# Kernel tuning notes

Hardware: AMD Instinct MI355X
Metric: run time of the kernel (lower is better)

The kernel has to match this reference:

```python
import jax, jax.numpy as jnp
import numpy as np
from jax import lax

B, DIM, RES = 1024, 384, 7
HEADS, KEY_DIM, ATTN_RATIO = 8, 32, 4
N = RES * RES            # 49
KH = KEY_DIM * HEADS     # 256
D = ATTN_RATIO * KEY_DIM # 128
DH = D * HEADS           # 1024
SCALE = KEY_DIM ** -0.5


def _rel_pos_idx():
    ii, jj = np.meshgrid(np.arange(RES), np.arange(RES), indexing='ij')
    pos = np.stack([ii.ravel(), jj.ravel()])          # [2, N]
    rel = np.abs(pos[:, :, None] - pos[:, None, :])   # [2, N, N]
    return jnp.asarray(rel[0] * RES + rel[1])         # [N, N] int

REL_IDX = _rel_pos_idx()


def conv1x1_bn(x, w, b, s, o):
    # 1x1 conv (pointwise GEMM) + eval-mode BatchNorm folded to scale/shift
    y = jnp.einsum('oc,bchw->bohw', w, x) + b[:, None, None]
    return y * s[:, None, None] + o[:, None, None]


def setup_inputs() -> dict:
    key = jax.random.key(0)
    ks = jax.random.split(key, 32)
    f = lambda i, shape, scale=0.02: jax.random.normal(ks[i], shape, jnp.float32) * scale
    u = lambda i, shape: jax.random.uniform(ks[i], shape, jnp.float32, 0.5, 1.5)
    inp = {
        'x': jax.random.normal(ks[0], (B, DIM, RES, RES), jnp.float32),
        'q_w': f(1, (KH, DIM)), 'q_b': f(2, (KH,)), 'q_s': u(3, (KH,)), 'q_o': f(4, (KH,)),
        'k_w': f(5, (KH, DIM)), 'k_b': f(6, (KH,)), 'k_s': u(7, (KH,)), 'k_o': f(8, (KH,)),
        'v_w': f(9, (DH, DIM)), 'v_b': f(10, (DH,)), 'v_s': u(11, (DH,)), 'v_o': f(12, (DH,)),
        'vl_w': f(13, (DH, 1, 3, 3)), 'vl_b': f(14, (DH,)), 'vl_s': u(15, (DH,)), 'vl_o': f(16, (DH,)),
        'th1_w': f(17, (HEADS, HEADS), 0.1), 'th1_b': f(18, (HEADS,)),
        'th2_w': f(19, (HEADS, HEADS), 0.1), 'th2_b': f(20, (HEADS,)),
        'p_w': f(21, (DIM, DH)), 'p_b': f(22, (DIM,)), 'p_s': u(23, (DIM,)), 'p_o': f(24, (DIM,)),
        'ab': f(25, (HEADS, N), 0.1),
    }
    return inp


def reference(x, q_w, q_b, q_s, q_o, k_w, k_b, k_s, k_o, v_w, v_b, v_s, v_o,
              vl_w, vl_b, vl_s, vl_o, th1_w, th1_b, th2_w, th2_b,
              p_w, p_b, p_s, p_o, ab):
    b = x.shape[0]
    q = conv1x1_bn(x, q_w, q_b, q_s, q_o).reshape(b, HEADS, KEY_DIM, N)
    q = q.transpose(0, 1, 3, 2)                         # [B,H,N,kd]
    k = conv1x1_bn(x, k_w, k_b, k_s, k_o).reshape(b, HEADS, KEY_DIM, N)  # [B,H,kd,N]
    v4 = conv1x1_bn(x, v_w, v_b, v_s, v_o)              # [B,DH,7,7]
    # local depthwise 3x3 branch + BN
    vl = lax.conv_general_dilated(v4, vl_w, (1, 1), 'SAME',
                                  feature_group_count=DH,
                                  dimension_numbers=('NCHW', 'OIHW', 'NCHW'))
    vl = (vl + vl_b[:, None, None]) * vl_s[:, None, None] + vl_o[:, None, None]
    v = v4.reshape(b, HEADS, D, N).transpose(0, 1, 3, 2)  # [B,H,N,d]

    bias = ab[:, REL_IDX]                                # [H,N,N]
    attn = jnp.einsum('bhnd,bhdm->bhnm', q, k) * SCALE + bias[None]
    # talking head 1 (1x1 conv over head dim)
    attn = jnp.einsum('ij,bjnm->binm', th1_w, attn) + th1_b[None, :, None, None]
    attn = jax.nn.softmax(attn, axis=-1)
    # talking head 2
    attn = jnp.einsum('ij,bjnm->binm', th2_w, attn) + th2_b[None, :, None, None]

    out = jnp.einsum('bhnm,bhmd->bhnd', attn, v)         # [B,H,N,d]
    out = out.transpose(0, 1, 3, 2).reshape(b, DH, RES, RES) + vl
    out = jax.nn.gelu(out, approximate=False)            # nn.GELU default = exact
    out = conv1x1_bn(out, p_w, p_b, p_s, p_o)            # [B,DIM,7,7]
    return out
```

## Files before the change

kernel.cpp:

```cpp
#include <hip/hip_runtime.h>
#include <math.h>

typedef unsigned short u16;
typedef unsigned int u32;
typedef short short8 __attribute__((ext_vector_type(8)));
typedef float f32x4 __attribute__((ext_vector_type(4)));
typedef unsigned int u32x2 __attribute__((ext_vector_type(2)));

#define SCALE_QK 0.17677669529663687f
#define PSLAB 23296

__device__ __forceinline__ float b2f(u16 v) { return __uint_as_float(((u32)v) << 16); }
__device__ __forceinline__ u16 f2b(float f) {
  u32 u = __float_as_uint(f);
  return (u16)((u + 0x7fffu + ((u >> 16) & 1u)) >> 16);
}

__device__ __forceinline__ float gelu_f(float z) {
  float y = z * 0.70710678118654752f;
  float a = fabsf(y);
  float t = __builtin_amdgcn_rcpf(fmaf(0.3275911f, a, 1.0f));
  float e = __expf(-y * y);
  float p = fmaf(1.061405429f, t, -1.453152027f);
  p = fmaf(p, t, 1.421413741f);
  p = fmaf(p, t, -0.284496736f);
  p = fmaf(p, t, 0.254829592f);
  p = p * t * e;
  float phi = (y >= 0.f) ? fmaf(-0.5f, p, 1.0f) : 0.5f * p;
  return z * phi;
}

__global__ __launch_bounds__(256) void k_pre(
    const float* __restrict__ th1w, const float* __restrict__ th1b, const float* __restrict__ ab,
    const float* __restrict__ qb, const float* __restrict__ qs, const float* __restrict__ qo,
    const float* __restrict__ kb, const float* __restrict__ ks, const float* __restrict__ ko,
    const float* __restrict__ vb, const float* __restrict__ vs, const float* __restrict__ vo,
    const float* __restrict__ pb, const float* __restrict__ ps, const float* __restrict__ po,
    const float* __restrict__ qw, const float* __restrict__ kw,
    const float* __restrict__ vw, const float* __restrict__ pw,
    float* __restrict__ bias2, float* __restrict__ alpha, float* __restrict__ beta,
    float* __restrict__ alphap, float* __restrict__ betap,
    u16* __restrict__ Wqk, u16* __restrict__ Wv, u16* __restrict__ Wp)
{
  int gid = blockIdx.x * 256 + threadIdx.x;
  if (gid < 19208) {
    int i = gid / 2401, rem = gid % 2401, n = rem / 49, m = rem % 49;
    int ry = abs(n / 7 - m / 7), rx = abs(n % 7 - m % 7);
    int idx = ry * 7 + rx;
    float acc = th1b[i];
    #pragma unroll
    for (int j = 0; j < 8; j++) acc += th1w[i * 8 + j] * ab[j * 49 + idx];
    bias2[gid] = acc;
  } else if (gid < 20744) {
    int c = gid - 19208;
    const float *s, *bb, *oo; int idx;
    if (c < 256)      { s = qs; bb = qb; oo = qo; idx = c; }
    else if (c < 512) { s = ks; bb = kb; oo = ko; idx = c - 256; }
    else              { s = vs; bb = vb; oo = vo; idx = c - 512; }
    float sv = s[idx];
    alpha[c] = sv;
    beta[c] = sv * bb[idx] + oo[idx];
  } else if (gid < 21128) {
    int c = gid - 20744;
    float sv = ps[c];
    alphap[c] = sv;
    betap[c] = sv * pb[c] + po[c];
  } else {
    int g = gid - 21128;
    if (g < 98304)       Wqk[g] = f2b(qw[g]);
    else if (g < 196608) Wqk[g] = f2b(kw[g - 98304]);
    else if (g < 589824) Wv[g - 196608] = f2b(vw[g - 196608]);
    else if (g < 983040) Wp[g - 589824] = f2b(pw[g - 589824]);
  }
}

__global__ __launch_bounds__(512, 4) void k_qk(
    const float* __restrict__ x, const u16* __restrict__ Wqk,
    const float* __restrict__ alpha, const float* __restrict__ beta,
    u16* __restrict__ Pbuf)
{
  __shared__ __align__(16) u16 lds[37376];
  u16* XT = lds;
  u16* Tq = lds + 26112;
  u16* Tk = lds + 31744;
  int t = threadIdx.x, wv = t >> 6, l = t & 63, quad = l >> 4, l16 = l & 15;
  int b = blockIdx.x;
  const float* xb = x + (size_t)b * 18816;

  for (int e = t; e < 18816; e += 512) {
    int k = e / 49, n = e - k * 49;
    XT[n * 408 + k] = f2b(xb[e]);
  }
  for (int e = t; e < 3060; e += 512) {
    int r = e / 204, kk = e - r * 204;
    ((u32*)(XT + (49 + r) * 408))[kk] = 0;
  }
  __syncthreads();

  u16* Pg = Pbuf + (size_t)b * PSLAB;
  int isK = wv >= 4, wl = wv & 3;
  for (int hp = 0; hp < 4; hp++) {
    int cbase = (isK ? 256 : 0) + hp * 64 + wl * 16;
    f32x4 acc[4] = {};
    const u16* Wr = Wqk + (size_t)(cbase + l16) * 384;
    short8 afr[12];
    #pragma unroll
    for (int ks = 0; ks < 12; ks++) afr[ks] = *(const short8*)(Wr + ks * 32 + quad * 8);
    #pragma unroll
    for (int ks = 0; ks < 12; ks++) {
      #pragma unroll
      for (int nt = 0; nt < 4; nt++) {
        short8 bf = *(const short8*)(&XT[(nt * 16 + l16) * 408 + ks * 32 + quad * 8]);
        acc[nt] = __builtin_amdgcn_mfma_f32_16x16x32_bf16(afr[ks], bf, acc[nt], 0, 0, 0);
      }
    }
    u16* Tdst = isK ? Tk : Tq;
    #pragma unroll
    for (int reg = 0; reg < 4; reg++) {
      int c = cbase + quad * 4 + reg;
      float al = alpha[c], be = beta[c];
      int cl = wl * 16 + quad * 4 + reg;
      #pragma unroll
      for (int nt = 0; nt < 4; nt++)
        Tdst[(nt * 16 + l16) * 88 + cl] = f2b(acc[nt][reg] * al + be);
    }
    __syncthreads();
    #pragma unroll
    for (int ui = 0; ui < 4; ui++) {
      int u = wv * 4 + ui;
      int hl = u >> 4, tn = (u >> 2) & 3, tm = u & 3;
      short8 a  = *(const short8*)(&Tq[(tn * 16 + l16) * 88 + hl * 32 + quad * 8]);
      short8 bb = *(const short8*)(&Tk[(tm * 16 + l16) * 88 + hl * 32 + quad * 8]);
      f32x4 c = {};
      c = __builtin_amdgcn_mfma_f32_16x16x32_bf16(a, bb, c, 0, 0, 0);
      int h = hp * 2 + hl;
      #pragma unroll
      for (int r = 0; r < 4; r++) {
        int n = tn * 16 + quad * 4 + r, m = tm * 16 + l16;
        if (n < 52 && m < 56)
          Pg[(h * 52 + n) * 56 + m] = (n < 49 && m < 49) ? f2b(c[r] * SCALE_QK) : (u16)0;
      }
    }
    __syncthreads();
  }
}

__global__ __launch_bounds__(256, 4) void k_mix(
    u16* __restrict__ Pbuf, const float* __restrict__ bias2,
    const float* __restrict__ th1w, const float* __restrict__ th1b,
    const float* __restrict__ th2w, const float* __restrict__ th2b)
{
  __shared__ u16 SB[23296];
  __shared__ float TH[144];
  int t = threadIdx.x, b = blockIdx.x;
  u32* Pg32 = (u32*)(Pbuf + (size_t)b * PSLAB);
  for (int e = t; e < 11648; e += 256) ((u32*)SB)[e] = Pg32[e];
  if (t < 64)       TH[t] = th1w[t];
  else if (t < 72)  TH[t] = th1b[t - 64];
  else if (t < 136) TH[t] = th2w[t - 72];
  else if (t < 144) TH[t] = th2b[t - 136];
  __syncthreads();
  for (int e = t; e < 2401; e += 256) {
    int n = e / 49, m = e - n * 49;
    float s[8], uo[8];
    #pragma unroll
    for (int j = 0; j < 8; j++) s[j] = b2f(SB[(j * 52 + n) * 56 + m]);
    #pragma unroll
    for (int i = 0; i < 8; i++) {
      float a2 = bias2[(i * 49 + n) * 49 + m];
      #pragma unroll
      for (int j = 0; j < 8; j++) a2 += TH[i * 8 + j] * s[j];
      uo[i] = a2;
    }
    #pragma unroll
    for (int i = 0; i < 8; i++) SB[(i * 52 + n) * 56 + m] = f2b(uo[i]);
  }
  __syncthreads();
  for (int r0 = t; r0 < 392; r0 += 256) {
    int i = r0 / 49, n = r0 - i * 49;
    u16* row = &SB[(i * 52 + n) * 56];
    float v[49]; float mx = -1e30f;
    #pragma unroll
    for (int m = 0; m < 49; m++) { v[m] = b2f(row[m]); mx = fmaxf(mx, v[m]); }
    float sum = 0.f;
    #pragma unroll
    for (int m = 0; m < 49; m++) { v[m] = __expf(v[m] - mx); sum += v[m]; }
    float inv = 1.f / sum;
    #pragma unroll
    for (int m = 0; m < 49; m++) row[m] = f2b(v[m] * inv);
  }
  __syncthreads();
  for (int e = t; e < 2401; e += 256) {
    int n = e / 49, m = e - n * 49;
    float s[8], uo[8];
    #pragma unroll
    for (int j = 0; j < 8; j++) s[j] = b2f(SB[(j * 52 + n) * 56 + m]);
    #pragma unroll
    for (int i = 0; i < 8; i++) {
      float a2 = TH[136 + i];
      #pragma unroll
      for (int j = 0; j < 8; j++) a2 += TH[72 + i * 8 + j] * s[j];
      uo[i] = a2;
    }
    #pragma unroll
    for (int i = 0; i < 8; i++) SB[(i * 52 + n) * 56 + m] = f2b(uo[i]);
  }
  __syncthreads();
  for (int e = t; e < 11648; e += 256) Pg32[e] = ((u32*)SB)[e];
}

__global__ __launch_bounds__(512, 4) void k_av(
    const float* __restrict__ x, const u16* __restrict__ Wv,
    const float* __restrict__ alpha, const float* __restrict__ beta,
    const float* __restrict__ vlw, const float* __restrict__ vlb,
    const float* __restrict__ vls, const float* __restrict__ vlo,
    const u16* __restrict__ Pbuf, u16* __restrict__ Zs)
{
  __shared__ __align__(16) u16 lds[38968];
  u16* XT = lds;
  u16* VT = lds + 26112;
  u16* Ph = lds + 35328;
  int t = threadIdx.x, wv = t >> 6, l = t & 63, quad = l >> 4, l16 = l & 15;
  int b = blockIdx.x;
  const float* xb = x + (size_t)b * 18816;

  for (int e = t; e < 18816; e += 512) {
    int k = e / 49, n = e - k * 49;
    XT[n * 408 + k] = f2b(xb[e]);
  }
  for (int e = t; e < 3060; e += 512) {
    int r = e / 204, kk = e - r * 204;
    ((u32*)(XT + (49 + r) * 408))[kk] = 0;
  }
  for (int e = t; e < 4608; e += 512) ((u32*)VT)[e] = 0;
  __syncthreads();

  u16* Zb = Zs + (size_t)b * 50176;
  const u16* Pgb = Pbuf + (size_t)b * PSLAB;
  for (int h = 0; h < 8; h++) {
    {
      const u32* src = (const u32*)(Pgb + h * 2912);
      for (int e = t; e < 1456; e += 512) ((u32*)Ph)[e] = src[e];
    }
    const u16* Wr = Wv + (size_t)(h * 128 + wv * 16 + l16) * 384;
    short8 afr[12];
    #pragma unroll
    for (int ks = 0; ks < 12; ks++) afr[ks] = *(const short8*)(Wr + ks * 32 + quad * 8);
    int d = wv * 16 + l16, c = h * 128 + d;
    float w9[9];
    #pragma unroll
    for (int j = 0; j < 9; j++) w9[j] = vlw[c * 9 + j];
    float sv = vls[c];
    float cb = sv * vlb[c] + vlo[c];

    f32x4 va[4] = {};
    #pragma unroll
    for (int ks = 0; ks < 12; ks++) {
      #pragma unroll
      for (int nt = 0; nt < 4; nt++) {
        short8 bf = *(const short8*)(&XT[(nt * 16 + l16) * 408 + ks * 32 + quad * 8]);
        va[nt] = __builtin_amdgcn_mfma_f32_16x16x32_bf16(afr[ks], bf, va[nt], 0, 0, 0);
      }
    }
    #pragma unroll
    for (int reg = 0; reg < 4; reg++) {
      int dl = wv * 16 + quad * 4 + reg;
      int cc = h * 128 + dl;
      float al = alpha[512 + cc], be = beta[512 + cc];
      #pragma unroll
      for (int nt = 0; nt < 4; nt++) {
        int m = nt * 16 + l16;
        if (m < 49) VT[dl * 72 + 8 + m] = f2b(va[nt][reg] * al + be);
      }
    }
    __syncthreads();
    f32x4 oa[4] = {};
    #pragma unroll
    for (int ks2 = 0; ks2 < 2; ks2++) {
      int mb = ks2 * 32 + quad * 8;
      short8 bf = *(const short8*)(&VT[(wv * 16 + l16) * 72 + 8 + mb]);
      #pragma unroll
      for (int tn = 0; tn < 4; tn++) {
        short8 af = *(const short8*)(&Ph[(tn * 16 + l16) * 56 + mb]);
        oa[tn] = __builtin_amdgcn_mfma_f32_16x16x32_bf16(af, bf, oa[tn], 0, 0, 0);
      }
    }
    const u16* vtr = &VT[d * 72];
    #pragma unroll
    for (int tn = 0; tn < 4; tn++) {
      int n0 = tn * 16 + quad * 4;
      const u16* vr = vtr + n0;
      float q[20];
      #pragma unroll
      for (int jj = 0; jj < 5; jj++) {
        u32x2 U = *(const u32x2*)(vr + jj * 4);
        q[jj * 4 + 0] = __uint_as_float(U.x << 16);
        q[jj * 4 + 1] = __uint_as_float(U.x & 0xffff0000u);
        q[jj * 4 + 2] = __uint_as_float(U.y << 16);
        q[jj * 4 + 3] = __uint_as_float(U.y & 0xffff0000u);
      }
      #pragma unroll
      for (int r = 0; r < 4; r++) {
        int n = n0 + r;
        int yi = (n * 37) >> 8;
        int xi = n - yi * 7;
        bool xl = xi > 0, xr = xi < 6;
        float w0m = xl ? w9[0] : 0.f, w3m = xl ? w9[3] : 0.f, w6m = xl ? w9[6] : 0.f;
        float w2m = xr ? w9[2] : 0.f, w5m = xr ? w9[5] : 0.f, w8m = xr ? w9[8] : 0.f;
        float conv = q[r]      * w0m + q[r + 1]  * w9[1] + q[r + 2]  * w2m
                   + q[r + 7]  * w3m + q[r + 8]  * w9[4] + q[r + 9]  * w5m
                   + q[r + 14] * w6m + q[r + 15] * w9[7] + q[r + 16] * w8m;
        float z = oa[tn][r] + conv * sv + cb;
        float g = gelu_f(z);
        if (n < 49) Zb[(size_t)n * 1024 + c] = f2b(g);
      }
    }
    __syncthreads();
  }
}

__global__ __launch_bounds__(512, 4) void k_proj(
    const u16* __restrict__ Wp, const u16* __restrict__ Zt,
    const float* __restrict__ alphap, const float* __restrict__ betap,
    float* __restrict__ out)
{
  __shared__ __align__(16) u16 Bs[128 * 152];
  int t = threadIdx.x, wv = t >> 6, l = t & 63, quad = l >> 4, l16 = l & 15;
  int g = blockIdx.x;
  int vb = (g & 7) * 192 + (g >> 3);
  int mb = vb % 3;
  size_t b0 = (size_t)(vb / 3) * 2;
  f32x4 acc[8] = {};
  const u16* Wr = Wp + (size_t)(mb * 128 + wv * 16 + l16) * 1024;
  for (int k0 = 0; k0 < 1024; k0 += 128) {
    #pragma unroll
    for (int i = 0; i < 4; i++) {
      int ch = t + i * 512;
      int np = ch >> 4, ck = ch & 15;
      int pb = np >> 6, n = np & 63;
      short8 v = {};
      if (n < 49)
        v = *(const short8*)(Zt + (b0 + pb) * 50176 + (size_t)n * 1024 + k0 + ck * 8);
      *(short8*)(&Bs[np * 152 + ck * 8]) = v;
    }
    __syncthreads();
    #pragma unroll
    for (int ksi = 0; ksi < 4; ksi++) {
      short8 af = *(const short8*)(Wr + k0 + ksi * 32 + quad * 8);
      #pragma unroll
      for (int nt = 0; nt < 8; nt++) {
        short8 bf = *(const short8*)(&Bs[(nt * 16 + l16) * 152 + ksi * 32 + quad * 8]);
        acc[nt] = __builtin_amdgcn_mfma_f32_16x16x32_bf16(af, bf, acc[nt], 0, 0, 0);
      }
    }
    __syncthreads();
  }
  #pragma unroll
  for (int reg = 0; reg < 4; reg++) {
    int c = mb * 128 + wv * 16 + quad * 4 + reg;
    float al = alphap[c], be = betap[c];
    #pragma unroll
    for (int nt = 0; nt < 8; nt++) {
      int np = nt * 16 + l16, pb = np >> 6, n = np & 63;
      if (n < 49) out[(b0 + pb) * 18816 + (size_t)c * 49 + n] = acc[nt][reg] * al + be;
    }
  }
}

extern "C" void kernel_launch(void* const* d_in, const int* in_sizes, int n_in,
                              void* d_out, int out_size, void* d_ws, size_t ws_size,
                              hipStream_t stream) {
  const float* x    = (const float*)d_in[0];
  const float* qw   = (const float*)d_in[1];
  const float* qb   = (const float*)d_in[2];
  const float* qs   = (const float*)d_in[3];
  const float* qo   = (const float*)d_in[4];
  const float* kw   = (const float*)d_in[5];
  const float* kb   = (const float*)d_in[6];
  const float* ks   = (const float*)d_in[7];
  const float* ko   = (const float*)d_in[8];
  const float* vw   = (const float*)d_in[9];
  const float* vb   = (const float*)d_in[10];
  const float* vs   = (const float*)d_in[11];
  const float* vo   = (const float*)d_in[12];
  const float* vlw  = (const float*)d_in[13];
  const float* vlb  = (const float*)d_in[14];
  const float* vls  = (const float*)d_in[15];
  const float* vlo  = (const float*)d_in[16];
  const float* th1w = (const float*)d_in[17];
  const float* th1b = (const float*)d_in[18];
  const float* th2w = (const float*)d_in[19];
  const float* th2b = (const float*)d_in[20];
  const float* pw   = (const float*)d_in[21];
  const float* pb   = (const float*)d_in[22];
  const float* ps   = (const float*)d_in[23];
  const float* po   = (const float*)d_in[24];
  const float* ab   = (const float*)d_in[25];
  float* out = (float*)d_out;
  char* ws = (char*)d_ws;

  u16* Pbuf = (u16*)d_out;

  float* bias2  = (float*)(ws + 0);
  float* alpha  = (float*)(ws + 77056);
  float* beta   = (float*)(ws + 83200);
  float* alphap = (float*)(ws + 89344);
  float* betap  = (float*)(ws + 90880);
  u16*   Wqk16  = (u16*)(ws + 92416);
  u16*   Wv16   = (u16*)(ws + 485632);
  u16*   Wp16   = (u16*)(ws + 1272064);
  u16*   Zs     = (u16*)(ws + 2058496);

  k_pre<<<3923, 256, 0, stream>>>(th1w, th1b, ab, qb, qs, qo, kb, ks, ko,
                                  vb, vs, vo, pb, ps, po, qw, kw, vw, pw,
                                  bias2, alpha, beta, alphap, betap,
                                  Wqk16, Wv16, Wp16);
  k_qk<<<1024, 512, 0, stream>>>(x, Wqk16, alpha, beta, Pbuf);
  k_mix<<<1024, 256, 0, stream>>>(Pbuf, bias2, th1w, th1b, th2w, th2b);
  k_av<<<1024, 512, 0, stream>>>(x, Wv16, alpha, beta, vlw, vlb, vls, vlo, Pbuf, Zs);
  k_proj<<<1536, 512, 0, stream>>>(Wp16, Zs, alphap, betap, out);
}
```

Baseline: 575.7 us.

## Reuse transposed bf16 x from k_qk in a split-head k_av kernel

k_qk now writes its transposed bf16 copy of x to a global workspace buffer. A new k_av_g kernel reads that buffer directly from global memory as MFMA operands instead of reconverting x into LDS. k_av_g also splits each batch across two blocks of four heads each, which cuts LDS use so more blocks can be resident at once. The cost is an extra global write and read of about 48KB per batch, and the path is only taken when the workspace is large enough; otherwise the old kernel runs.

```diff
diff --git a/kernel.cpp b/kernel.cpp
--- a/kernel.cpp
+++ b/kernel.cpp
@@ -77,7 +77,7 @@
 __global__ __launch_bounds__(512, 4) void k_qk(
     const float* __restrict__ x, const u16* __restrict__ Wqk,
     const float* __restrict__ alpha, const float* __restrict__ beta,
-    u16* __restrict__ Pbuf)
+    u16* __restrict__ Pbuf, u16* __restrict__ XTg)
 {
   __shared__ __align__(16) u16 lds[37376];
   u16* XT = lds;
@@ -96,6 +96,15 @@
     ((u32*)(XT + (49 + r) * 408))[kk] = 0;
   }
   __syncthreads();
+
+  if (XTg) {
+    u32* dst = (u32*)(XTg + (size_t)b * 24576);
+    const u32* src32 = (const u32*)XT;
+    for (int e = t; e < 12288; e += 512) {
+      int row = e / 192, cc = e - row * 192;
+      dst[e] = src32[row * 204 + cc];
+    }
+  }
 
   u16* Pg = Pbuf + (size_t)b * PSLAB;
   int isK = wv >= 4, wl = wv & 3;
@@ -209,7 +218,113 @@
   for (int e = t; e < 11648; e += 256) Pg32[e] = ((u32*)SB)[e];
 }
 
-__global__ __launch_bounds__(512, 4) void k_av(
+__global__ __launch_bounds__(512, 8) void k_av_g(
+    const u16* __restrict__ XTg, const u16* __restrict__ Wv,
+    const float* __restrict__ alpha, const float* __restrict__ beta,
+    const float* __restrict__ vlw, const float* __restrict__ vlb,
+    const float* __restrict__ vls, const float* __restrict__ vlo,
+    const u16* __restrict__ Pbuf, u16* __restrict__ Zs)
+{
+  __shared__ __align__(16) u16 lds[12856];
+  u16* VT = lds;
+  u16* Ph = lds + 9216;
+  int t = threadIdx.x, wv = t >> 6, l = t & 63, quad = l >> 4, l16 = l & 15;
+  int bid = blockIdx.x;
+  int b = bid >> 1, h0 = (bid & 1) * 4;
+  const u16* XTb = XTg + (size_t)b * 24576;
+  u16* Zb = Zs + (size_t)b * 50176;
+  const u16* Pgb = Pbuf + (size_t)b * PSLAB;
+  int d = wv * 16 + l16;
+
+  for (int e = t; e < 4608; e += 512) ((u32*)VT)[e] = 0;
+
+  const u16* xr0 = XTb + (0 * 16 + l16) * 384 + quad * 8;
+  const u16* xr1 = XTb + (1 * 16 + l16) * 384 + quad * 8;
+  const u16* xr2 = XTb + (2 * 16 + l16) * 384 + quad * 8;
+  const u16* xr3 = XTb + (3 * 16 + l16) * 384 + quad * 8;
+  __syncthreads();
+
+  for (int hh = 0; hh < 4; hh++) {
+    int h = h0 + hh;
+    int c = h * 128 + d;
+    {
+      const u32* src = (const u32*)(Pgb + h * 2912);
+      u32* dst = (u32*)Ph;
+      for (int e = t; e < 1456; e += 512) dst[e] = src[e];
+    }
+    const u16* Wr = Wv + (size_t)c * 384 + quad * 8;
+    f32x4 va[4] = {};
+    #pragma unroll
+    for (int ks = 0; ks < 12; ks++) {
+      short8 af = *(const short8*)(Wr + ks * 32);
+      va[0] = __builtin_amdgcn_mfma_f32_16x16x32_bf16(af, *(const short8*)(xr0 + ks * 32), va[0], 0, 0, 0);
+      va[1] = __builtin_amdgcn_mfma_f32_16x16x32_bf16(af, *(const short8*)(xr1 + ks * 32), va[1], 0, 0, 0);
+      va[2] = __builtin_amdgcn_mfma_f32_16x16x32_bf16(af, *(const short8*)(xr2 + ks * 32), va[2], 0, 0, 0);
+      va[3] = __builtin_amdgcn_mfma_f32_16x16x32_bf16(af, *(const short8*)(xr3 + ks * 32), va[3], 0, 0, 0);
+    }
+    #pragma unroll
+    for (int reg = 0; reg < 4; reg++) {
+      int dl = wv * 16 + quad * 4 + reg;
+      int cc = h * 128 + dl;
+      float al = alpha[512 + cc], be = beta[512 + cc];
+      #pragma unroll
+      for (int nt = 0; nt < 4; nt++) {
+        int m = nt * 16 + l16;
+        if (m < 49) VT[dl * 72 + 8 + m] = f2b(va[nt][reg] * al + be);
+      }
+    }
+    __syncthreads();
+    float w9[9];
+    #pragma unroll
+    for (int j = 0; j < 9; j++) w9[j] = vlw[c * 9 + j];
+    float sv = vls[c];
+    float cb = sv * vlb[c] + vlo[c];
+    f32x4 oa[4] = {};
+    #pragma unroll
+    for (int ks2 = 0; ks2 < 2; ks2++) {
+      int mb = ks2 * 32 + quad * 8;
+      short8 bf = *(const short8*)(&VT[(wv * 16 + l16) * 72 + 8 + mb]);
+      #pragma unroll
+      for (int tn = 0; tn < 4; tn++) {
+        short8 af = *(const short8*)(&Ph[(tn * 16 + l16) * 56 + mb]);
+        oa[tn] = __builtin_amdgcn_mfma_f32_16x16x32_bf16(af, bf, oa[tn], 0, 0, 0);
+      }
+    }
+    const u16* vtr = &VT[d * 72];
+    #pragma unroll
+    for (int tn = 0; tn < 4; tn++) {
+      int n0 = tn * 16 + quad * 4;
+      const u16* vr = vtr + n0;
+      float q[20];
+      #pragma unroll
+      for (int jj = 0; jj < 5; jj++) {
+        u32x2 U = *(const u32x2*)(vr + jj * 4);
+        q[jj * 4 + 0] = __uint_as_float(U.x << 16);
+        q[jj * 4 + 1] = __uint_as_float(U.x & 0xffff0000u);
+        q[jj * 4 + 2] = __uint_as_float(U.y << 16);
+        q[jj * 4 + 3] = __uint_as_float(U.y & 0xffff0000u);
+      }
+      #pragma unroll
+      for (int r = 0; r < 4; r++) {
+        int n = n0 + r;
+        int yi = (n * 37) >> 8;
+        int xi = n - yi * 7;
+        bool xl = xi > 0, xr = xi < 6;
+        float w0m = xl ? w9[0] : 0.f, w3m = xl ? w9[3] : 0.f, w6m = xl ? w9[6] : 0.f;
+        float w2m = xr ? w9[2] : 0.f, w5m = xr ? w9[5] : 0.f, w8m = xr ? w9[8] : 0.f;
+        float conv = q[r]      * w0m + q[r + 1]  * w9[1] + q[r + 2]  * w2m
+                   + q[r + 7]  * w3m + q[r + 8]  * w9[4] + q[r + 9]  * w5m
+                   + q[r + 14] * w6m + q[r + 15] * w9[7] + q[r + 16] * w8m;
+        float z = oa[tn][r] + conv * sv + cb;
+        float g = gelu_f(z);
+        if (n < 49) Zb[(size_t)n * 1024 + c] = f2b(g);
+      }
+    }
+    __syncthreads();
+  }
+}
+
+__global__ __launch_bounds__(512, 4) void k_av_fb(
     const float* __restrict__ x, const u16* __restrict__ Wv,
     const float* __restrict__ alpha, const float* __restrict__ beta,
     const float* __restrict__ vlw, const float* __restrict__ vlb,
@@ -410,13 +525,18 @@
   u16*   Wv16   = (u16*)(ws + 485632);
   u16*   Wp16   = (u16*)(ws + 1272064);
   u16*   Zs     = (u16*)(ws + 2058496);
+  bool big = ws_size >= 155150592ull;
+  u16*   XTg    = big ? (u16*)(ws + 104818944) : (u16*)nullptr;
 
   k_pre<<<3923, 256, 0, stream>>>(th1w, th1b, ab, qb, qs, qo, kb, ks, ko,
                                   vb, vs, vo, pb, ps, po, qw, kw, vw, pw,
                                   bias2, alpha, beta, alphap, betap,
                                   Wqk16, Wv16, Wp16);
-  k_qk<<<1024, 512, 0, stream>>>(x, Wqk16, alpha, beta, Pbuf);
+  k_qk<<<1024, 512, 0, stream>>>(x, Wqk16, alpha, beta, Pbuf, XTg);
   k_mix<<<1024, 256, 0, stream>>>(Pbuf, bias2, th1w, th1b, th2w, th2b);
-  k_av<<<1024, 512, 0, stream>>>(x, Wv16, alpha, beta, vlw, vlb, vls, vlo, Pbuf, Zs);
+  if (big)
+    k_av_g<<<2048, 512, 0, stream>>>(XTg, Wv16, alpha, beta, vlw, vlb, vls, vlo, Pbuf, Zs);
+  else
+    k_av_fb<<<1024, 512, 0, stream>>>(x, Wv16, alpha, beta, vlw, vlb, vls, vlo, Pbuf, Zs);
   k_proj<<<1536, 512, 0, stream>>>(Wp16, Zs, alphap, betap, out);
 }
```

Result: slower. 1.634 ms (+183.7%).
